# Kernel optimization log

Measured on AMD Instinct MI355X. Metric: run time of the kernel, lower is better.

Reference implementation:

```python
import jax, jax.numpy as jnp
import numpy as np

DN = ('NCDHW', 'OIDHW', 'NCDHW')

def conv3(x, w):
    # 3x3x3 VALID stencil conv: [1,1,D+2,H+2,W+2] -> [1,1,D,H,W]
    return jax.lax.conv_general_dilated(x, w, (1, 1, 1), 'VALID', dimension_numbers=DN)

def conv_res(x, w):
    # 2x2x2 stride-2 restriction
    return jax.lax.conv_general_dilated(x, w, (2, 2, 2), 'VALID', dimension_numbers=DN)

def prol(x):
    for ax in (2, 3, 4):
        x = jnp.repeat(x, 2, axis=ax)
    return x

def with_halo(x, factor=1.0):
    # apply_BC_* + halo_exchange on one device: edge-replicate a 1-cell halo,
    # optionally scaled by `factor` (apply_BC_u uses -1.0 -> no-slip wall).
    p = jnp.pad(x, ((0, 0), (0, 0), (1, 1), (1, 1), (1, 1)), mode='edge')
    if factor != 1.0:
        interior = jnp.pad(jnp.ones_like(x), ((0, 0), (0, 0), (1, 1), (1, 1), (1, 1)))
        p = p * (interior + factor * (1.0 - interior))
    return p

def pad0(x):
    # apply_BC_cw: zero halo for the multigrid correction
    return jnp.pad(x, ((0, 0), (0, 0), (1, 1), (1, 1), (1, 1)))


def setup_inputs() -> dict:
    key = jax.random.key(0)
    ks = jax.random.split(key, 12)
    D = 128
    shp = (1, 1, D, D, D)
    f32 = jnp.float32
    values_u = jax.random.normal(ks[0], shp, f32)
    values_v = jax.random.normal(ks[1], shp, f32)
    values_w = jax.random.normal(ks[2], shp, f32)
    values_p = jax.random.normal(ks[3], shp, f32)
    sigma = jax.random.uniform(ks[4], shp, f32)
    kshape = (1, 1, 3, 3, 3)
    w_xadv = 0.1 * jax.random.normal(ks[5], kshape, f32)
    w_yadv = 0.1 * jax.random.normal(ks[6], kshape, f32)
    w_zadv = 0.1 * jax.random.normal(ks[7], kshape, f32)
    w_diff = 0.1 * jax.random.normal(ks[8], kshape, f32)
    wA = 0.1 * jax.random.normal(ks[9], kshape, f32)
    wA = wA.at[0, 0, 1, 1, 1].add(-6.0)  # Laplacian-like diagonal so Jacobi division is stable
    w_res = 0.1 * jax.random.normal(ks[10], (1, 1, 2, 2, 2), f32)
    dt = 0.05 * jnp.ones((1,), f32)
    return dict(values_u=values_u, values_v=values_v, values_w=values_w,
                values_p=values_p, sigma=sigma, w_xadv=w_xadv, w_yadv=w_yadv,
                w_zadv=w_zadv, w_diff=w_diff, wA=wA, w_res=w_res, dt=dt,
                iteration=2, nlevel=9)


def reference(values_u, values_v, values_w, values_p, sigma, w_xadv, w_yadv,
              w_zadv, w_diff, wA, w_res, dt, iteration, nlevel):
    diag = wA[0, 0, 1, 1, 1]
    xadv = lambda t: conv3(t, w_xadv)
    yadv = lambda t: conv3(t, w_yadv)
    zadv = lambda t: conv3(t, w_zadv)
    diff = lambda t: conv3(t, w_diff)
    A = lambda t: conv3(t, wA)

    def solid(a, b, c):
        d = 1.0 + dt * sigma
        return a / d, b / d, c / d

    def PG(uu, vv, ww, u, v, w):
        # k_u/k_v/k_w are ones; k_uu/k_vv/k_ww are their BC+halo versions (also ones)
        k_h = with_halo(jnp.ones_like(u))
        k_u = 0.5 * (diff(uu) + diff(uu * k_h) - u * diff(k_h))
        k_v = 0.5 * (diff(vv) + diff(vv * k_h) - v * diff(k_h))
        k_w = 0.5 * (diff(ww) + diff(ww * k_h) - w * diff(k_h))
        return k_u, k_v, k_w

    def f_cycle_mg(uu, vv, wwh, p, pp):
        b = -(xadv(uu) + yadv(vv) + zadv(wwh)) / dt
        w_mg = jnp.zeros((1, 1, 1, 1, 1), p.dtype)
        r = b
        for _ in range(iteration):
            w_mg = jnp.zeros((1, 1, 1, 1, 1), p.dtype)
            r = A(pp) - b
            r_s = [r]
            for _i in range(1, nlevel - 1):
                r = conv_res(r, w_res)
                r_s.append(r)
            for i in reversed(range(1, nlevel - 1)):
                ww_ = pad0(w_mg)
                w_mg = w_mg - A(ww_) / diag + r_s[i] / diag
                w_mg = prol(w_mg)
            p = p - w_mg
            p = p - A(pp) / diag + b / diag
            pp = with_halo(p)
        return p, w_mg, r, pp

    u, v, w = solid(values_u, values_v, values_w)
    uu = with_halo(u, -1.0)
    vv = with_halo(v)
    wwh = with_halo(w)
    pp = with_halo(values_p)

    k_u, k_v, k_w = PG(uu, vv, wwh, u, v, w)
    b_u = u + 0.5 * (0.001 * k_u * dt - u * xadv(uu) * dt - v * yadv(uu) * dt - w * zadv(uu) * dt) - xadv(pp) * dt
    b_v = v + 0.5 * (0.001 * k_v * dt - u * xadv(vv) * dt - v * yadv(vv) * dt - w * zadv(vv) * dt) - yadv(pp) * dt
    b_w = w + 0.5 * (0.001 * k_w * dt - u * xadv(wwh) * dt - v * yadv(wwh) * dt - w * zadv(wwh) * dt) - zadv(pp) * dt
    b_u, b_v, b_w = solid(b_u, b_v, b_w)
    b_uu = with_halo(b_u, -1.0)
    b_vv = with_halo(b_v)
    b_ww = with_halo(b_w)

    k_u, k_v, k_w = PG(b_uu, b_vv, b_ww, b_u, b_v, b_w)
    u = u + 0.001 * k_u * dt - b_u * xadv(b_uu) * dt - b_v * yadv(b_uu) * dt - b_w * zadv(b_uu) * dt - xadv(pp) * dt
    v = v + 0.001 * k_v * dt - b_u * xadv(b_vv) * dt - b_v * yadv(b_vv) * dt - b_w * zadv(b_vv) * dt - yadv(pp) * dt
    w = w + 0.001 * k_w * dt - b_u * xadv(b_ww) * dt - b_v * yadv(b_ww) * dt - b_w * zadv(b_ww) * dt - zadv(pp) * dt
    u, v, w = solid(u, v, w)

    uu = with_halo(u, -1.0)
    vv = with_halo(v)
    wwh = with_halo(w)
    p, w_mg, r, pp = f_cycle_mg(uu, vv, wwh, values_p, pp)

    u = u - xadv(pp) * dt
    v = v - yadv(pp) * dt
    w = w - zadv(pp) * dt
    u, v, w = solid(u, v, w)
    return (u, v, w, p, w_mg, r)
```

## Files before the change

### kernel.cpp

```cpp
#include <hip/hip_runtime.h>


#define NN 128
#define NF (NN*NN*NN)


__device__ __forceinline__ void prep9(int z, int y, int rb[9], bool rn[9]) {
  int zi[3] = {z > 0 ? z-1 : 0, z, z < NN-1 ? z+1 : NN-1};
  int yi[3] = {y > 0 ? y-1 : 0, y, y < NN-1 ? y+1 : NN-1};
  bool zo[3] = {z == 0, false, z == NN-1};
  bool yo[3] = {y == 0, false, y == NN-1};
#pragma unroll
  for (int a = 0; a < 3; ++a)
#pragma unroll
    for (int b = 0; b < 3; ++b) {
      rb[a*3+b] = (zi[a]*NN + yi[b])*NN;
      rn[a*3+b] = zo[a] | yo[b];
    }
}

template<bool NEG>
__device__ __forceinline__ void sten4(
    const float* __restrict__ f, const int rb[9], const bool rn[9],
    bool lo, bool hi, int x0,
    const float* __restrict__ w0p, const float* __restrict__ w1p,
    const float* __restrict__ w2p, const float* __restrict__ w3p,
    float acc[4][4], float4* center) {
  const float* const Ws[4] = {w0p, w1p, w2p, w3p};
#pragma unroll
  for (int r = 0; r < 9; ++r) {
    int base = rb[r] + x0;
    float4 c = *(const float4*)(f + base);
    float m1 = f[base - (lo ? 0 : 1)];
    float p4 = f[base + (hi ? 3 : 4)];
    if (NEG) {
      float sr = rn[r] ? -1.f : 1.f;
      m1 *= (rn[r] | lo) ? -1.f : 1.f;
      p4 *= (rn[r] | hi) ? -1.f : 1.f;
      c.x *= sr; c.y *= sr; c.z *= sr; c.w *= sr;
    }
    if (r == 4 && center) *center = c;
    float t[6] = {m1, c.x, c.y, c.z, c.w, p4};
#pragma unroll
    for (int s = 0; s < 4; ++s) {
      const float* W = Ws[s];
      float a0 = W[r*3+0], a1 = W[r*3+1], a2 = W[r*3+2];
#pragma unroll
      for (int k = 0; k < 4; ++k)
        acc[s][k] = fmaf(a0, t[k], fmaf(a1, t[k+1], fmaf(a2, t[k+2], acc[s][k])));
    }
  }
}

__device__ __forceinline__ void sten_p3(
    const float* __restrict__ f, const int rb[9],
    bool lo, bool hi, int x0,
    const float* __restrict__ w0p, const float* __restrict__ w1p,
    const float* __restrict__ w2p, float acc[3][4]) {
  const float* const Ws[3] = {w0p, w1p, w2p};
#pragma unroll
  for (int r = 0; r < 9; ++r) {
    int base = rb[r] + x0;
    float4 c = *(const float4*)(f + base);
    float m1 = f[base - (lo ? 0 : 1)];
    float p4 = f[base + (hi ? 3 : 4)];
    float t[6] = {m1, c.x, c.y, c.z, c.w, p4};
#pragma unroll
    for (int s = 0; s < 3; ++s) {
      const float* W = Ws[s];
      float a0 = W[r*3+0], a1 = W[r*3+1], a2 = W[r*3+2];
#pragma unroll
      for (int k = 0; k < 4; ++k)
        acc[s][k] = fmaf(a0, t[k], fmaf(a1, t[k+1], fmaf(a2, t[k+2], acc[s][k])));
    }
  }
}


__global__ void __launch_bounds__(256) k_prep(
    float* __restrict__ uo, float* __restrict__ vo, float* __restrict__ wo,
    float* __restrict__ gqu, float* __restrict__ gqv, float* __restrict__ gqw,
    float* __restrict__ ap0,
    const float* __restrict__ vu, const float* __restrict__ vv, const float* __restrict__ vw,
    const float* __restrict__ pf, const float* __restrict__ sg,
    const float* __restrict__ wx, const float* __restrict__ wy,
    const float* __restrict__ wz, const float* __restrict__ wA,
    const float* __restrict__ dtp) {
  int x0 = threadIdx.x * 4;
  int y  = blockIdx.x * 8 + threadIdx.y;
  int z  = blockIdx.y;
  bool lo = (x0 == 0), hi = (x0 == NN-4);
  int rb[9]; bool rn[9];
  prep9(z, y, rb, rn);
  float dt = dtp[0];
  int i4 = ((z*NN + y)*NN + x0) >> 2;

  float4 u4 = ((const float4*)vu)[i4];
  float4 v4 = ((const float4*)vv)[i4];
  float4 w4 = ((const float4*)vw)[i4];
  float4 s4 = ((const float4*)sg)[i4];

  float aP[4][4] = {};
  sten4<false>(pf, rb, rn, lo, hi, x0, wx, wy, wz, wA, aP, (float4*)nullptr);

  float uv[4] = {u4.x, u4.y, u4.z, u4.w};
  float vv_[4] = {v4.x, v4.y, v4.z, v4.w};
  float wv[4] = {w4.x, w4.y, w4.z, w4.w};
  float sv[4] = {s4.x, s4.y, s4.z, s4.w};
  float ou[4], ov[4], ow[4], gu[4], gv[4], gw[4];
#pragma unroll
  for (int k = 0; k < 4; ++k) {
    float rd = 1.0f / (1.0f + dt*sv[k]);
    ou[k] = uv[k]*rd; ov[k] = vv_[k]*rd; ow[k] = wv[k]*rd;
    gu[k] = ou[k] - aP[0][k]*dt;
    gv[k] = ov[k] - aP[1][k]*dt;
    gw[k] = ow[k] - aP[2][k]*dt;
  }
  ((float4*)uo)[i4]  = make_float4(ou[0], ou[1], ou[2], ou[3]);
  ((float4*)vo)[i4]  = make_float4(ov[0], ov[1], ov[2], ov[3]);
  ((float4*)wo)[i4]  = make_float4(ow[0], ow[1], ow[2], ow[3]);
  ((float4*)gqu)[i4] = make_float4(gu[0], gu[1], gu[2], gu[3]);
  ((float4*)gqv)[i4] = make_float4(gv[0], gv[1], gv[2], gv[3]);
  ((float4*)gqw)[i4] = make_float4(gw[0], gw[1], gw[2], gw[3]);
  ((float4*)ap0)[i4] = make_float4(aP[3][0], aP[3][1], aP[3][2], aP[3][3]);
}

__global__ void __launch_bounds__(256) k_mom3(
    float* __restrict__ du, float* __restrict__ dv, float* __restrict__ dw,
    const float* __restrict__ su, const float* __restrict__ sv, const float* __restrict__ sw,
    const float* __restrict__ gqu, const float* __restrict__ gqv, const float* __restrict__ gqw,
    const float* __restrict__ sg,
    const float* __restrict__ wx, const float* __restrict__ wy,
    const float* __restrict__ wz, const float* __restrict__ wd,
    const float* __restrict__ dtp, float scale) {
  int x0 = threadIdx.x * 4;
  int y  = blockIdx.x * 8 + threadIdx.y;
  int z  = blockIdx.y;
  bool lo = (x0 == 0), hi = (x0 == NN-4);
  int rb[9]; bool rn[9];
  prep9(z, y, rb, rn);
  float dt = dtp[0];
  int i4 = ((z*NN + y)*NN + x0) >> 2;

  float4 gu4 = ((const float4*)gqu)[i4];
  float4 gv4 = ((const float4*)gqv)[i4];
  float4 gw4 = ((const float4*)gqw)[i4];
  float4 sg4 = ((const float4*)sg)[i4];

  float aU[4][4] = {}, aV[4][4] = {}, aW[4][4] = {};
  float4 uc, vc, wc;
  sten4<true >(su, rb, rn, lo, hi, x0, wx, wy, wz, wd, aU, &uc);
  sten4<false>(sv, rb, rn, lo, hi, x0, wx, wy, wz, wd, aV, &vc);
  sten4<false>(sw, rb, rn, lo, hi, x0, wx, wy, wz, wd, aW, &wc);

  float sw27 = 0.f;
#pragma unroll
  for (int j = 0; j < 27; ++j) sw27 += wd[j];

  float ucv[4] = {uc.x, uc.y, uc.z, uc.w};
  float vcv[4] = {vc.x, vc.y, vc.z, vc.w};
  float wcv[4] = {wc.x, wc.y, wc.z, wc.w};
  float guv[4] = {gu4.x, gu4.y, gu4.z, gu4.w};
  float gvv[4] = {gv4.x, gv4.y, gv4.z, gv4.w};
  float gwv[4] = {gw4.x, gw4.y, gw4.z, gw4.w};
  float sgv[4] = {sg4.x, sg4.y, sg4.z, sg4.w};
  float ou[4], ov[4], ow[4];
#pragma unroll
  for (int k = 0; k < 4; ++k) {
    float ku = aU[3][k] - 0.5f*sw27*ucv[k];
    float kv = aV[3][k] - 0.5f*sw27*vcv[k];
    float kw = aW[3][k] - 0.5f*sw27*wcv[k];
    float ru = guv[k] + scale*dt*(0.001f*ku - ucv[k]*aU[0][k] - vcv[k]*aU[1][k] - wcv[k]*aU[2][k]);
    float rv = gvv[k] + scale*dt*(0.001f*kv - ucv[k]*aV[0][k] - vcv[k]*aV[1][k] - wcv[k]*aV[2][k]);
    float rw = gwv[k] + scale*dt*(0.001f*kw - ucv[k]*aW[0][k] - vcv[k]*aW[1][k] - wcv[k]*aW[2][k]);
    float rd = 1.0f / (1.0f + dt*sgv[k]);
    ou[k] = ru*rd; ov[k] = rv*rd; ow[k] = rw*rd;
  }
  ((float4*)du)[i4] = make_float4(ou[0], ou[1], ou[2], ou[3]);
  ((float4*)dv)[i4] = make_float4(ov[0], ov[1], ov[2], ov[3]);
  ((float4*)dw)[i4] = make_float4(ow[0], ow[1], ow[2], ow[3]);
}


__device__ __forceinline__ void row4(const float* __restrict__ f, int base,
                                     bool lo, bool hi, float t[4]) {
  float2 c = *(const float2*)(f + base);
  t[0] = f[base - (lo ? 0 : 1)];
  t[1] = c.x; t[2] = c.y;
  t[3] = f[base + (hi ? 1 : 2)];
}

__device__ __forceinline__ void prep16(int Z, int Y, int rb[16], bool rn[16]) {
  int z0 = 2*Z, y0 = 2*Y;
  int zi[4] = {z0 > 0 ? z0-1 : 0, z0, z0+1, z0+2 < NN ? z0+2 : NN-1};
  int yi[4] = {y0 > 0 ? y0-1 : 0, y0, y0+1, y0+2 < NN ? y0+2 : NN-1};
  bool zo[4] = {Z == 0, false, false, Z == 63};
  bool yo[4] = {Y == 0, false, false, Y == 63};
#pragma unroll
  for (int a = 0; a < 4; ++a)
#pragma unroll
    for (int b = 0; b < 4; ++b) {
      rb[a*4+b] = (zi[a]*NN + yi[b])*NN;
      rn[a*4+b] = zo[a] | yo[b];
    }
}

template<bool NEG>
__device__ __forceinline__ void cc_acc(
    const float* __restrict__ f, const float* __restrict__ W,
    const int rb[16], const bool rn[16], bool lo, bool hi, int x0,
    float out8[8]) {
#pragma unroll
  for (int zp = 0; zp < 4; ++zp) {
    float t[4][4];
#pragma unroll
    for (int yp = 0; yp < 4; ++yp) {
      row4(f, rb[zp*4+yp] + x0, lo, hi, t[yp]);
      if (NEG) {
        bool rno = rn[zp*4+yp];
        float sr = rno ? -1.f : 1.f;
        t[yp][1] *= sr; t[yp][2] *= sr;
        t[yp][0] *= (rno | lo) ? -1.f : 1.f;
        t[yp][3] *= (rno | hi) ? -1.f : 1.f;
      }
    }
#pragma unroll
    for (int dz = 0; dz < 2; ++dz) {
      int a = zp - dz;
      if (a < 0 || a > 2) continue;
#pragma unroll
      for (int oy = 0; oy < 2; ++oy)
#pragma unroll
        for (int b = 0; b < 3; ++b) {
          const float* tr = t[oy + b];
          float w0 = W[(a*3+b)*3+0], w1 = W[(a*3+b)*3+1], w2 = W[(a*3+b)*3+2];
#pragma unroll
          for (int dx = 0; dx < 2; ++dx)
            out8[(dz*2+oy)*2+dx] =
              fmaf(w0, tr[dx], fmaf(w1, tr[dx+1], fmaf(w2, tr[dx+2], out8[(dz*2+oy)*2+dx])));
        }
    }
  }
}

__global__ void __launch_bounds__(256) k_bdivres0(
    float* __restrict__ bb, float* __restrict__ rfine, float* __restrict__ rc1,
    const float* __restrict__ su, const float* __restrict__ sv, const float* __restrict__ sw,
    const float* __restrict__ ap0,
    const float* __restrict__ wx, const float* __restrict__ wy, const float* __restrict__ wz,
    const float* __restrict__ wr, const float* __restrict__ dtp) {
  int i = blockIdx.x*256 + threadIdx.x;
  if (i >= 64*64*64) return;
  int X = i & 63, Y = (i >> 6) & 63, Z = i >> 12;
  bool lo = (X == 0), hi = (X == 63);
  int x0 = 2*X;
  int rb[16]; bool rn[16];
  prep16(Z, Y, rb, rn);
  float rdt = 1.0f / dtp[0];

  float s8[8] = {};
  cc_acc<true >(su, wx, rb, rn, lo, hi, x0, s8);
  cc_acc<false>(sv, wy, rb, rn, lo, hi, x0, s8);
  cc_acc<false>(sw, wz, rb, rn, lo, hi, x0, s8);

  float rsum = 0.f;
#pragma unroll
  for (int dz = 0; dz < 2; ++dz)
#pragma unroll
    for (int oy = 0; oy < 2; ++oy) {
      int fi = ((2*Z+dz)*NN + (2*Y+oy))*NN + x0;
      float2 a2 = *(const float2*)(ap0 + fi);
      float av[2] = {a2.x, a2.y};
#pragma unroll
      for (int dx = 0; dx < 2; ++dx) {
        int f = (dz*2+oy)*2+dx;
        float bcell = -s8[f] * rdt;
        float rcell = av[dx] - bcell;
        bb[fi+dx] = bcell;
        rfine[fi+dx] = rcell;
        rsum = fmaf(wr[f], rcell, rsum);
      }
    }
  rc1[i] = rsum;
}

__global__ void __launch_bounds__(256) k_resres1(
    float* __restrict__ rfine, float* __restrict__ rc1,
    const float* __restrict__ pf, const float* __restrict__ bb,
    const float* __restrict__ wA, const float* __restrict__ wr) {
  int i = blockIdx.x*256 + threadIdx.x;
  if (i >= 64*64*64) return;
  int X = i & 63, Y = (i >> 6) & 63, Z = i >> 12;
  bool lo = (X == 0), hi = (X == 63);
  int x0 = 2*X;
  int rb[16]; bool rn[16];
  prep16(Z, Y, rb, rn);
  float a8[8] = {};
  cc_acc<false>(pf, wA, rb, rn, lo, hi, x0, a8);
  float rsum = 0.f;
#pragma unroll
  for (int f = 0; f < 8; ++f) {
    int dz = f >> 2, dy = (f >> 1) & 1, dx = f & 1;
    int idx = ((2*Z+dz)*NN + (2*Y+dy))*NN + x0 + dx;
    float rcell = a8[f] - bb[idx];
    rfine[idx] = rcell;
    rsum = fmaf(wr[(dz*2+dy)*2+dx], rcell, rsum);
  }
  rc1[i] = rsum;
}

__global__ void __launch_bounds__(256) k_restrict(
    float* __restrict__ dst, const float* __restrict__ src,
    const float* __restrict__ wr, int no) {
  int i = blockIdx.x*256 + threadIdx.x;
  int n3 = no*no*no;
  if (i >= n3) return;
  int x = i % no; int t = i / no; int y = t % no; int z = t / no;
  int ni = 2*no;
  float s = 0.f;
#pragma unroll
  for (int a = 0; a < 2; ++a)
#pragma unroll
    for (int b = 0; b < 2; ++b)
#pragma unroll
      for (int c = 0; c < 2; ++c)
        s = fmaf(wr[(a*2+b)*2+c], src[((2*z+a)*ni + (2*y+b))*ni + (2*x+c)], s);
  dst[i] = s;
}

__device__ __forceinline__ float azb_prol(const float* __restrict__ wh, int hs, int s,
    int z, int y, int x, const float* __restrict__ wA) {
  float acc = 0.f;
#pragma unroll
  for (int a = 0; a < 3; ++a) { int zz = z + a - 1; if ((unsigned)zz >= (unsigned)s) continue;
#pragma unroll
    for (int b = 0; b < 3; ++b) { int yy = y + b - 1; if ((unsigned)yy >= (unsigned)s) continue;
#pragma unroll
      for (int c = 0; c < 3; ++c) { int xx = x + c - 1; if ((unsigned)xx >= (unsigned)s) continue;
        acc = fmaf(wA[(a*3+b)*3+c], wh[((zz>>1)*hs + (yy>>1))*hs + (xx>>1)], acc);
      } } }
  return acc;
}

__global__ void __launch_bounds__(512) k_mg_small(
    float* __restrict__ w16, float* __restrict__ r_o,
    const float* __restrict__ rc2,
    const float* __restrict__ wA, const float* __restrict__ wr) {
  __shared__ float r16[4096];
  __shared__ float r8[512];
  __shared__ float r4[64];
  __shared__ float r2[8];
  __shared__ float wa[512];
  __shared__ float wb[64];
  __shared__ float scal[2];
  int tid = threadIdx.x;
  float diag = wA[13];
  float wrl[8];
#pragma unroll
  for (int j = 0; j < 8; ++j) wrl[j] = wr[j];

  for (int j = tid; j < 4096; j += 512) {
    int x = j & 15, y = (j >> 4) & 15, z = j >> 8;
    float s = 0.f;
#pragma unroll
    for (int a = 0; a < 2; ++a)
#pragma unroll
      for (int b = 0; b < 2; ++b)
#pragma unroll
        for (int c = 0; c < 2; ++c)
          s = fmaf(wrl[(a*2+b)*2+c], rc2[((2*z+a)*32 + (2*y+b))*32 + (2*x+c)], s);
    r16[j] = s;
  }
  __syncthreads();
  {
    int j = tid;
    int x = j & 7, y = (j >> 3) & 7, z = j >> 6;
    float s = 0.f;
#pragma unroll
    for (int a = 0; a < 2; ++a)
#pragma unroll
      for (int b = 0; b < 2; ++b)
#pragma unroll
        for (int c = 0; c < 2; ++c)
          s = fmaf(wrl[(a*2+b)*2+c], r16[((2*z+a)*16 + (2*y+b))*16 + (2*x+c)], s);
    r8[j] = s;
  }
  __syncthreads();
  if (tid < 64) {
    int x = tid & 3, y = (tid >> 2) & 3, z = tid >> 4;
    float s = 0.f;
#pragma unroll
    for (int a = 0; a < 2; ++a)
#pragma unroll
      for (int b = 0; b < 2; ++b)
#pragma unroll
        for (int c = 0; c < 2; ++c)
          s = fmaf(wrl[(a*2+b)*2+c], r8[((2*z+a)*8 + (2*y+b))*8 + (2*x+c)], s);
    r4[tid] = s;
  }
  __syncthreads();
  if (tid < 8) {
    int x = tid & 1, y = (tid >> 1) & 1, z = tid >> 2;
    float s = 0.f;
#pragma unroll
    for (int a = 0; a < 2; ++a)
#pragma unroll
      for (int b = 0; b < 2; ++b)
#pragma unroll
        for (int c = 0; c < 2; ++c)
          s = fmaf(wrl[(a*2+b)*2+c], r4[((2*z+a)*4 + (2*y+b))*4 + (2*x+c)], s);
    r2[tid] = s;
  }
  __syncthreads();
  if (tid == 0) {
    float s = 0.f;
#pragma unroll
    for (int j = 0; j < 8; ++j) s = fmaf(wrl[j], r2[j], s);
    scal[0] = s;
    r_o[0] = s;
    scal[1] = s / diag;
  }
  __syncthreads();
  if (tid < 8) {
    int x = tid & 1, y = (tid >> 1) & 1, z = tid >> 2;
    float wp = scal[1];
    float az = azb_prol(&scal[1], 1, 2, z, y, x, wA);
    wa[tid] = wp - az/diag + r2[tid]/diag;
  }
  __syncthreads();
  if (tid < 64) {
    int x = tid & 3, y = (tid >> 2) & 3, z = tid >> 4;
    float wp = wa[((z>>1)*2 + (y>>1))*2 + (x>>1)];
    float az = azb_prol(wa, 2, 4, z, y, x, wA);
    wb[tid] = wp - az/diag + r4[tid]/diag;
  }
  __syncthreads();
  {
    int j = tid;
    int x = j & 7, y = (j >> 3) & 7, z = j >> 6;
    float wp = wb[((z>>1)*4 + (y>>1))*4 + (x>>1)];
    float az = azb_prol(wb, 4, 8, z, y, x, wA);
    wa[j] = wp - az/diag + r8[j]/diag;
  }
  __syncthreads();
  for (int j = tid; j < 4096; j += 512) {
    int x = j & 15, y = (j >> 4) & 15, z = j >> 8;
    float wp = wa[((z>>1)*8 + (y>>1))*8 + (x>>1)];
    float az = azb_prol(wa, 8, 16, z, y, x, wA);
    w16[j] = wp - az/diag + r16[j]/diag;
  }
}

__global__ void __launch_bounds__(256) k_coarse_step(
    float* __restrict__ wout, const float* __restrict__ wh,
    const float* __restrict__ rl, const float* __restrict__ wA, int s) {
  int i = blockIdx.x*256 + threadIdx.x;
  int n3 = s*s*s;
  if (i >= n3) return;
  int x = i % s; int t = i / s; int y = t % s; int z = t / s;
  int hs = s >> 1;
  float diag = wA[13];
  float wp = wh[((z>>1)*hs + (y>>1))*hs + (x>>1)];
  float az = azb_prol(wh, hs, s, z, y, x, wA);
  wout[i] = wp - az/diag + rl[i]/diag;
}

__global__ void __launch_bounds__(256) k_pupd4(
    float* __restrict__ pdst, float* __restrict__ wmgo,
    const float* __restrict__ psrc, const float* __restrict__ rfine,
    const float* __restrict__ w64, const float* __restrict__ wA, int writeWmg) {
  int i4 = blockIdx.x*256 + threadIdx.x;
  if (i4 >= NF/4) return;
  int i = i4*4;
  int x = i & (NN-1); int t = i >> 7; int y = t & (NN-1); int z = t >> 7;
  float rdiag = 1.0f / wA[13];
  float2 w2 = *(const float2*)(w64 + ((size_t)(z>>1)*64 + (y>>1))*64 + (x>>1));
  float4 ps = ((const float4*)psrc)[i4];
  float4 rf = ((const float4*)rfine)[i4];
  float4 o = make_float4(ps.x - w2.x - rf.x*rdiag,
                         ps.y - w2.x - rf.y*rdiag,
                         ps.z - w2.y - rf.z*rdiag,
                         ps.w - w2.y - rf.w*rdiag);
  ((float4*)pdst)[i4] = o;
  if (writeWmg) ((float4*)wmgo)[i4] = make_float4(w2.x, w2.x, w2.y, w2.y);
}

__global__ void __launch_bounds__(256) k_proj3(
    float* __restrict__ u, float* __restrict__ v, float* __restrict__ w,
    const float* __restrict__ pf, const float* __restrict__ sg,
    const float* __restrict__ wx, const float* __restrict__ wy,
    const float* __restrict__ wz, const float* __restrict__ dtp) {
  int x0 = threadIdx.x * 4;
  int y  = blockIdx.x * 8 + threadIdx.y;
  int z  = blockIdx.y;
  bool lo = (x0 == 0), hi = (x0 == NN-4);
  int rb[9]; bool rn[9];
  prep9(z, y, rb, rn);
  float aP[3][4] = {};
  sten_p3(pf, rb, lo, hi, x0, wx, wy, wz, aP);
  float dt = dtp[0];
  int i4 = ((z*NN + y)*NN + x0) >> 2;
  float4 u4 = ((const float4*)u)[i4];
  float4 v4 = ((const float4*)v)[i4];
  float4 w4 = ((const float4*)w)[i4];
  float4 sg4 = ((const float4*)sg)[i4];
  float ua[4] = {u4.x, u4.y, u4.z, u4.w};
  float va[4] = {v4.x, v4.y, v4.z, v4.w};
  float wa[4] = {w4.x, w4.y, w4.z, w4.w};
  float sa[4] = {sg4.x, sg4.y, sg4.z, sg4.w};
  float ou[4], ov[4], ow[4];
#pragma unroll
  for (int k = 0; k < 4; ++k) {
    float rd = 1.0f / (1.0f + dt*sa[k]);
    ou[k] = (ua[k] - aP[0][k]*dt)*rd;
    ov[k] = (va[k] - aP[1][k]*dt)*rd;
    ow[k] = (wa[k] - aP[2][k]*dt)*rd;
  }
  ((float4*)u)[i4] = make_float4(ou[0], ou[1], ou[2], ou[3]);
  ((float4*)v)[i4] = make_float4(ov[0], ov[1], ov[2], ov[3]);
  ((float4*)w)[i4] = make_float4(ow[0], ow[1], ow[2], ow[3]);
}


extern "C" void kernel_launch(void* const* d_in, const int* in_sizes, int n_in,
                              void* d_out, int out_size, void* d_ws, size_t ws_size,
                              hipStream_t stream) {
  const float* values_u = (const float*)d_in[0];
  const float* values_v = (const float*)d_in[1];
  const float* values_w = (const float*)d_in[2];
  const float* values_p = (const float*)d_in[3];
  const float* sigma    = (const float*)d_in[4];
  const float* wx       = (const float*)d_in[5];
  const float* wy       = (const float*)d_in[6];
  const float* wz       = (const float*)d_in[7];
  const float* wd       = (const float*)d_in[8];
  const float* wA       = (const float*)d_in[9];
  const float* wr       = (const float*)d_in[10];
  const float* dtp      = (const float*)d_in[11];

  float* out   = (float*)d_out;
  float* u_o   = out;
  float* v_o   = out + (size_t)NF;
  float* w_o   = out + (size_t)2*NF;
  float* p_o   = out + (size_t)3*NF;
  float* wmg_o = out + (size_t)4*NF;
  float* r_o   = out + (size_t)5*NF;

  float* ws    = (float*)d_ws;
  float* f0    = ws;
  float* f1    = f0 + (size_t)NF;
  float* f2    = f1 + (size_t)NF;
  float* bws   = f2 + (size_t)NF;
  float* rfine = bws + (size_t)NF;
  float* pbuf  = rfine + (size_t)NF;
  float* gqu   = pbuf + (size_t)NF;
  float* gqv   = gqu + (size_t)NF;
  float* gqw   = gqv + (size_t)NF;
  float* ap0   = gqw + (size_t)NF;
  float* rc1   = ap0 + (size_t)NF;
  float* rc2   = rc1 + 262144;
  float* w16   = rc2 + 32768;
  float* w32   = w16 + 4096;
  float* w64   = w32 + 32768;

  const int TB = 256;
  dim3 blkS(32, 8, 1);
  dim3 grdS(16, 128, 1);

  k_prep<<<grdS, blkS, 0, stream>>>(u_o, v_o, w_o, gqu, gqv, gqw, ap0,
                                    values_u, values_v, values_w, values_p, sigma,
                                    wx, wy, wz, wA, dtp);
  k_mom3<<<grdS, blkS, 0, stream>>>(f0, f1, f2, u_o, v_o, w_o, gqu, gqv, gqw,
                                    sigma, wx, wy, wz, wd, dtp, 0.5f);
  k_mom3<<<grdS, blkS, 0, stream>>>(u_o, v_o, w_o, f0, f1, f2, gqu, gqv, gqw,
                                    sigma, wx, wy, wz, wd, dtp, 1.0f);

  k_bdivres0<<<1024, TB, 0, stream>>>(bws, rfine, rc1, u_o, v_o, w_o, ap0,
                                      wx, wy, wz, wr, dtp);
  k_restrict<<<128, TB, 0, stream>>>(rc2, rc1, wr, 32);
  k_mg_small<<<1, 512, 0, stream>>>(w16, r_o, rc2, wA, wr);
  k_coarse_step<<<128, TB, 0, stream>>>(w32, w16, rc2, wA, 32);
  k_coarse_step<<<1024, TB, 0, stream>>>(w64, w32, rc1, wA, 64);
  k_pupd4<<<NF/4/TB, TB, 0, stream>>>(pbuf, wmg_o, values_p, rfine, w64, wA, 0);

  k_resres1<<<1024, TB, 0, stream>>>(rfine, rc1, pbuf, bws, wA, wr);
  k_restrict<<<128, TB, 0, stream>>>(rc2, rc1, wr, 32);
  k_mg_small<<<1, 512, 0, stream>>>(w16, r_o, rc2, wA, wr);
  k_coarse_step<<<128, TB, 0, stream>>>(w32, w16, rc2, wA, 32);
  k_coarse_step<<<1024, TB, 0, stream>>>(w64, w32, rc1, wA, 64);
  k_pupd4<<<NF/4/TB, TB, 0, stream>>>(p_o, wmg_o, pbuf, rfine, w64, wA, 1);

  k_proj3<<<grdS, blkS, 0, stream>>>(u_o, v_o, w_o, p_o, sigma, wx, wy, wz, dtp);
}
```

Baseline: 226.3 us.

## Stage momentum and divergence stencils through LDS rolling z-plane slabs

The momentum and divergence stencil kernels now stage three-field halo planes into shared memory and march each block through four z-planes with a rolling four-slot buffer. Neighbour values are read from LDS instead of being re-read from global or cache by every thread. The divergence kernel no longer fuses the 2x restriction, so an extra k_restrict launch over the fine grid now produces rc1. This trades redundant global loads for about 63 KB of LDS per block, two barriers per plane, fewer blocks, and an extra pass over rfine.

Result: slower. 302.2 us (+33.6%).

```diff
diff --git a/kernel.cpp b/kernel.cpp
--- a/kernel.cpp
+++ b/kernel.cpp
@@ -3,6 +3,48 @@
 
 #define NN 128
 #define NF (NN*NN*NN)
+
+#define YB 8
+#define ZSEG 4
+#define SLABW 132
+#define SLABROWS 10
+#define SLABF (SLABROWS*SLABW)
+#define SLAB3 (3*SLABF)
+
+
+template<bool NEGU>
+__device__ __forceinline__ void stage_plane(
+    float* __restrict__ slab,
+    int zp, int y0,
+    const float* __restrict__ su, const float* __restrict__ sv,
+    const float* __restrict__ sw, int tid) {
+  int slot = (zp + 4) & 3;
+  int gz = zp < 0 ? 0 : (zp > NN-1 ? NN-1 : zp);
+  bool zoob = (zp < 0) | (zp > NN-1);
+  float* sbase = slab + (size_t)slot * SLAB3;
+#pragma unroll
+  for (int it = 0; it < 16; ++it) {
+    int j = tid + it*256;
+    if (j >= SLAB3) break;
+    int f  = j / SLABF;
+    int rem = j - f*SLABF;
+    int ry = rem / SLABW;
+    int rx = rem - ry*SLABW;
+    if (rx < 130) {
+      int ly = y0 - 1 + ry;
+      int lx = rx - 1;
+      int gy = ly < 0 ? 0 : (ly > NN-1 ? NN-1 : ly);
+      int gx = lx < 0 ? 0 : (lx > NN-1 ? NN-1 : lx);
+      const float* fp = (f == 0) ? su : ((f == 1) ? sv : sw);
+      float v = fp[(gz*NN + gy)*NN + gx];
+      if (NEGU && f == 0) {
+        bool oob = zoob | (ly < 0) | (ly > NN-1) | (lx < 0) | (lx > NN-1);
+        v = oob ? -v : v;
+      }
+      sbase[f*SLABF + ry*SLABW + rx] = v;
+    }
+  }
+}
 
 
 __device__ __forceinline__ void prep9(int z, int y, int rb[9], bool rn[9]) {
@@ -75,7 +117,6 @@
     }
   }
 }
-
 
 __global__ void __launch_bounds__(256) k_prep(
     float* __restrict__ uo, float* __restrict__ vo, float* __restrict__ wo,
@@ -125,7 +166,7 @@
   ((float4*)ap0)[i4] = make_float4(aP[3][0], aP[3][1], aP[3][2], aP[3][3]);
 }
 
-__global__ void __launch_bounds__(256) k_mom3(
+__global__ void __launch_bounds__(256) k_mom3_lds(
     float* __restrict__ du, float* __restrict__ dv, float* __restrict__ dw,
     const float* __restrict__ su, const float* __restrict__ sv, const float* __restrict__ sw,
     const float* __restrict__ gqu, const float* __restrict__ gqv, const float* __restrict__ gqw,
@@ -133,52 +174,143 @@
     const float* __restrict__ wx, const float* __restrict__ wy,
     const float* __restrict__ wz, const float* __restrict__ wd,
     const float* __restrict__ dtp, float scale) {
-  int x0 = threadIdx.x * 4;
-  int y  = blockIdx.x * 8 + threadIdx.y;
-  int z  = blockIdx.y;
-  bool lo = (x0 == 0), hi = (x0 == NN-4);
-  int rb[9]; bool rn[9];
-  prep9(z, y, rb, rn);
+  __shared__ float slab[4*SLAB3];
+  int tid = threadIdx.y*32 + threadIdx.x;
+  int xq = threadIdx.x, yy = threadIdx.y;
+  int x0 = xq*4;
+  int y0 = blockIdx.x * YB;
+  int z0 = blockIdx.y * ZSEG;
+  int y  = y0 + yy;
   float dt = dtp[0];
-  int i4 = ((z*NN + y)*NN + x0) >> 2;
-
-  float4 gu4 = ((const float4*)gqu)[i4];
-  float4 gv4 = ((const float4*)gqv)[i4];
-  float4 gw4 = ((const float4*)gqw)[i4];
-  float4 sg4 = ((const float4*)sg)[i4];
-
-  float aU[4][4] = {}, aV[4][4] = {}, aW[4][4] = {};
-  float4 uc, vc, wc;
-  sten4<true >(su, rb, rn, lo, hi, x0, wx, wy, wz, wd, aU, &uc);
-  sten4<false>(sv, rb, rn, lo, hi, x0, wx, wy, wz, wd, aV, &vc);
-  sten4<false>(sw, rb, rn, lo, hi, x0, wx, wy, wz, wd, aW, &wc);
+  const float* Ws[4] = {wx, wy, wz, wd};
 
   float sw27 = 0.f;
 #pragma unroll
   for (int j = 0; j < 27; ++j) sw27 += wd[j];
 
-  float ucv[4] = {uc.x, uc.y, uc.z, uc.w};
-  float vcv[4] = {vc.x, vc.y, vc.z, vc.w};
-  float wcv[4] = {wc.x, wc.y, wc.z, wc.w};
-  float guv[4] = {gu4.x, gu4.y, gu4.z, gu4.w};
-  float gvv[4] = {gv4.x, gv4.y, gv4.z, gv4.w};
-  float gwv[4] = {gw4.x, gw4.y, gw4.z, gw4.w};
-  float sgv[4] = {sg4.x, sg4.y, sg4.z, sg4.w};
-  float ou[4], ov[4], ow[4];
-#pragma unroll
-  for (int k = 0; k < 4; ++k) {
-    float ku = aU[3][k] - 0.5f*sw27*ucv[k];
-    float kv = aV[3][k] - 0.5f*sw27*vcv[k];
-    float kw = aW[3][k] - 0.5f*sw27*wcv[k];
-    float ru = guv[k] + scale*dt*(0.001f*ku - ucv[k]*aU[0][k] - vcv[k]*aU[1][k] - wcv[k]*aU[2][k]);
-    float rv = gvv[k] + scale*dt*(0.001f*kv - ucv[k]*aV[0][k] - vcv[k]*aV[1][k] - wcv[k]*aV[2][k]);
-    float rw = gwv[k] + scale*dt*(0.001f*kw - ucv[k]*aW[0][k] - vcv[k]*aW[1][k] - wcv[k]*aW[2][k]);
-    float rd = 1.0f / (1.0f + dt*sgv[k]);
-    ou[k] = ru*rd; ov[k] = rv*rd; ow[k] = rw*rd;
-  }
-  ((float4*)du)[i4] = make_float4(ou[0], ou[1], ou[2], ou[3]);
-  ((float4*)dv)[i4] = make_float4(ov[0], ov[1], ov[2], ov[3]);
-  ((float4*)dw)[i4] = make_float4(ow[0], ow[1], ow[2], ow[3]);
+  stage_plane<true>(slab, z0-1, y0, su, sv, sw, tid);
+  stage_plane<true>(slab, z0,   y0, su, sv, sw, tid);
+
+  for (int z = z0; z < z0 + ZSEG; ++z) {
+    stage_plane<true>(slab, z+1, y0, su, sv, sw, tid);
+    __syncthreads();
+
+    float aF[3][4][4] = {};
+    float cen[3][4];
+#pragma unroll
+    for (int f = 0; f < 3; ++f) {
+#pragma unroll
+      for (int dz = 0; dz < 3; ++dz) {
+        int slot = (z-1+dz + 4) & 3;
+        const float* fb = slab + (size_t)slot*SLAB3 + f*SLABF;
+#pragma unroll
+        for (int dy = 0; dy < 3; ++dy) {
+          const float* row = fb + (yy+dy)*SLABW + x0;
+          float4 A = *(const float4*)row;
+          float2 B = *(const float2*)(row + 4);
+          float t[6] = {A.x, A.y, A.z, A.w, B.x, B.y};
+          if (dz == 1 && dy == 1) {
+            cen[f][0] = t[1]; cen[f][1] = t[2]; cen[f][2] = t[3]; cen[f][3] = t[4];
+          }
+#pragma unroll
+          for (int s = 0; s < 4; ++s) {
+            const float* W = Ws[s];
+            float a0 = W[(dz*3+dy)*3+0], a1 = W[(dz*3+dy)*3+1], a2 = W[(dz*3+dy)*3+2];
+#pragma unroll
+            for (int k = 0; k < 4; ++k)
+              aF[f][s][k] = fmaf(a0, t[k], fmaf(a1, t[k+1], fmaf(a2, t[k+2], aF[f][s][k])));
+          }
+        }
+      }
+    }
+
+    int i4 = ((z*NN + y)*NN + x0) >> 2;
+    float4 gu4 = ((const float4*)gqu)[i4];
+    float4 gv4 = ((const float4*)gqv)[i4];
+    float4 gw4 = ((const float4*)gqw)[i4];
+    float4 sg4 = ((const float4*)sg)[i4];
+    float guv[4] = {gu4.x, gu4.y, gu4.z, gu4.w};
+    float gvv[4] = {gv4.x, gv4.y, gv4.z, gv4.w};
+    float gwv[4] = {gw4.x, gw4.y, gw4.z, gw4.w};
+    float sgv[4] = {sg4.x, sg4.y, sg4.z, sg4.w};
+    float ou[4], ov[4], ow[4];
+#pragma unroll
+    for (int k = 0; k < 4; ++k) {
+      float cu = cen[0][k], cv = cen[1][k], cw = cen[2][k];
+      float ku = aF[0][3][k] - 0.5f*sw27*cu;
+      float kv = aF[1][3][k] - 0.5f*sw27*cv;
+      float kw = aF[2][3][k] - 0.5f*sw27*cw;
+      float ru = guv[k] + scale*dt*(0.001f*ku - cu*aF[0][0][k] - cv*aF[0][1][k] - cw*aF[0][2][k]);
+      float rv = gvv[k] + scale*dt*(0.001f*kv - cu*aF[1][0][k] - cv*aF[1][1][k] - cw*aF[1][2][k]);
+      float rw = gwv[k] + scale*dt*(0.001f*kw - cu*aF[2][0][k] - cv*aF[2][1][k] - cw*aF[2][2][k]);
+      float rd = 1.0f / (1.0f + dt*sgv[k]);
+      ou[k] = ru*rd; ov[k] = rv*rd; ow[k] = rw*rd;
+    }
+    ((float4*)du)[i4] = make_float4(ou[0], ou[1], ou[2], ou[3]);
+    ((float4*)dv)[i4] = make_float4(ov[0], ov[1], ov[2], ov[3]);
+    ((float4*)dw)[i4] = make_float4(ow[0], ow[1], ow[2], ow[3]);
+    __syncthreads();
+  }
+}
+
+__global__ void __launch_bounds__(256) k_bdiv_lds(
+    float* __restrict__ bb, float* __restrict__ rfine,
+    const float* __restrict__ su, const float* __restrict__ sv, const float* __restrict__ sw,
+    const float* __restrict__ ap0,
+    const float* __restrict__ wx, const float* __restrict__ wy, const float* __restrict__ wz,
+    const float* __restrict__ dtp) {
+  __shared__ float slab[4*SLAB3];
+  int tid = threadIdx.y*32 + threadIdx.x;
+  int xq = threadIdx.x, yy = threadIdx.y;
+  int x0 = xq*4;
+  int y0 = blockIdx.x * YB;
+  int z0 = blockIdx.y * ZSEG;
+  int y  = y0 + yy;
+  float rdt = 1.0f / dtp[0];
+  const float* Ws[3] = {wx, wy, wz};
+
+  stage_plane<true>(slab, z0-1, y0, su, sv, sw, tid);
+  stage_plane<true>(slab, z0,   y0, su, sv, sw, tid);
+
+  for (int z = z0; z < z0 + ZSEG; ++z) {
+    stage_plane<true>(slab, z+1, y0, su, sv, sw, tid);
+    __syncthreads();
+
+    float sacc[4] = {};
+#pragma unroll
+    for (int f = 0; f < 3; ++f) {
+      const float* W = Ws[f];
+#pragma unroll
+      for (int dz = 0; dz < 3; ++dz) {
+        int slot = (z-1+dz + 4) & 3;
+        const float* fb = slab + (size_t)slot*SLAB3 + f*SLABF;
+#pragma unroll
+        for (int dy = 0; dy < 3; ++dy) {
+          const float* row = fb + (yy+dy)*SLABW + x0;
+          float4 A = *(const float4*)row;
+          float2 B = *(const float2*)(row + 4);
+          float t[6] = {A.x, A.y, A.z, A.w, B.x, B.y};
+          float a0 = W[(dz*3+dy)*3+0], a1 = W[(dz*3+dy)*3+1], a2 = W[(dz*3+dy)*3+2];
+#pragma unroll
+          for (int k = 0; k < 4; ++k)
+            sacc[k] = fmaf(a0, t[k], fmaf(a1, t[k+1], fmaf(a2, t[k+2], sacc[k])));
+        }
+      }
+    }
+
+    int i4 = ((z*NN + y)*NN + x0) >> 2;
+    float4 a4 = ((const float4*)ap0)[i4];
+    float av[4] = {a4.x, a4.y, a4.z, a4.w};
+    float bv[4], rv[4];
+#pragma unroll
+    for (int k = 0; k < 4; ++k) {
+      bv[k] = -sacc[k]*rdt;
+      rv[k] = av[k] - bv[k];
+    }
+    ((float4*)bb)[i4]    = make_float4(bv[0], bv[1], bv[2], bv[3]);
+    ((float4*)rfine)[i4] = make_float4(rv[0], rv[1], rv[2], rv[3]);
+    __syncthreads();
+  }
 }
 
 
@@ -241,47 +373,6 @@
         }
     }
   }
-}
-
-__global__ void __launch_bounds__(256) k_bdivres0(
-    float* __restrict__ bb, float* __restrict__ rfine, float* __restrict__ rc1,
-    const float* __restrict__ su, const float* __restrict__ sv, const float* __restrict__ sw,
-    const float* __restrict__ ap0,
-    const float* __restrict__ wx, const float* __restrict__ wy, const float* __restrict__ wz,
-    const float* __restrict__ wr, const float* __restrict__ dtp) {
-  int i = blockIdx.x*256 + threadIdx.x;
-  if (i >= 64*64*64) return;
-  int X = i & 63, Y = (i >> 6) & 63, Z = i >> 12;
-  bool lo = (X == 0), hi = (X == 63);
-  int x0 = 2*X;
-  int rb[16]; bool rn[16];
-  prep16(Z, Y, rb, rn);
-  float rdt = 1.0f / dtp[0];
-
-  float s8[8] = {};
-  cc_acc<true >(su, wx, rb, rn, lo, hi, x0, s8);
-  cc_acc<false>(sv, wy, rb, rn, lo, hi, x0, s8);
-  cc_acc<false>(sw, wz, rb, rn, lo, hi, x0, s8);
-
-  float rsum = 0.f;
-#pragma unroll
-  for (int dz = 0; dz < 2; ++dz)
-#pragma unroll
-    for (int oy = 0; oy < 2; ++oy) {
-      int fi = ((2*Z+dz)*NN + (2*Y+oy))*NN + x0;
-      float2 a2 = *(const float2*)(ap0 + fi);
-      float av[2] = {a2.x, a2.y};
-#pragma unroll
-      for (int dx = 0; dx < 2; ++dx) {
-        int f = (dz*2+oy)*2+dx;
-        float bcell = -s8[f] * rdt;
-        float rcell = av[dx] - bcell;
-        bb[fi+dx] = bcell;
-        rfine[fi+dx] = rcell;
-        rsum = fmaf(wr[f], rcell, rsum);
-      }
-    }
-  rc1[i] = rsum;
 }
 
 __global__ void __launch_bounds__(256) k_resres1(
@@ -566,17 +657,20 @@
   const int TB = 256;
   dim3 blkS(32, 8, 1);
   dim3 grdS(16, 128, 1);
+  dim3 blkM(32, 8, 1);
+  dim3 grdM(16, 32, 1);
 
   k_prep<<<grdS, blkS, 0, stream>>>(u_o, v_o, w_o, gqu, gqv, gqw, ap0,
                                     values_u, values_v, values_w, values_p, sigma,
                                     wx, wy, wz, wA, dtp);
-  k_mom3<<<grdS, blkS, 0, stream>>>(f0, f1, f2, u_o, v_o, w_o, gqu, gqv, gqw,
-                                    sigma, wx, wy, wz, wd, dtp, 0.5f);
-  k_mom3<<<grdS, blkS, 0, stream>>>(u_o, v_o, w_o, f0, f1, f2, gqu, gqv, gqw,
-                                    sigma, wx, wy, wz, wd, dtp, 1.0f);
-
-  k_bdivres0<<<1024, TB, 0, stream>>>(bws, rfine, rc1, u_o, v_o, w_o, ap0,
-                                      wx, wy, wz, wr, dtp);
+  k_mom3_lds<<<grdM, blkM, 0, stream>>>(f0, f1, f2, u_o, v_o, w_o, gqu, gqv, gqw,
+                                        sigma, wx, wy, wz, wd, dtp, 0.5f);
+  k_mom3_lds<<<grdM, blkM, 0, stream>>>(u_o, v_o, w_o, f0, f1, f2, gqu, gqv, gqw,
+                                        sigma, wx, wy, wz, wd, dtp, 1.0f);
+
+  k_bdiv_lds<<<grdM, blkM, 0, stream>>>(bws, rfine, u_o, v_o, w_o, ap0,
+                                        wx, wy, wz, dtp);
+  k_restrict<<<1024, TB, 0, stream>>>(rc1, rfine, wr, 64);
   k_restrict<<<128, TB, 0, stream>>>(rc2, rc1, wr, 32);
   k_mg_small<<<1, 512, 0, stream>>>(w16, r_o, rc2, wA, wr);
   k_coarse_step<<<128, TB, 0, stream>>>(w32, w16, rc2, wA, 32);
```
